# Optimization experiments

Hardware: AMD Instinct MI355X
Metric: run time of the kernel (lower is better)

Reference implementation:

```python
import jax, jax.numpy as jnp
import numpy as np

N = 8192
F_IN = 64
F_OUT = 64
ALPHA = 0.2  # LeakyReLU negative slope
NEG_INF = -9e15


def setup_inputs() -> dict:
    key = jax.random.key(0)
    k1, k2, k3, k4 = jax.random.split(key, 4)
    h = jax.random.normal(k1, (N, F_IN), dtype=jnp.float32)
    adj = jax.random.randint(k2, (N, N), 0, 2, dtype=jnp.int32)
    W = jax.random.normal(k3, (F_OUT, F_IN), dtype=jnp.float32) * (1.0 / np.sqrt(F_IN))
    a = jax.random.normal(k4, (2 * F_OUT,), dtype=jnp.float32) * (1.0 / np.sqrt(2 * F_OUT))
    return {"h": h, "adj": adj, "W": W, "a": a}


def reference(h, adj, W, a):
    # Wh = h @ W.T  (nn.Linear with no bias)
    Wh = h @ W.T  # [N, F_out]
    # The original builds [N*N, 2F] pairs then applies `a`; this is exactly
    # e_ij = leakyrelu(a1 . Wh_i + a2 . Wh_j) -- decomposed form, same math.
    a1, a2 = a[:F_OUT], a[F_OUT:]
    src = Wh @ a1  # [N]
    dst = Wh @ a2  # [N]
    e = jax.nn.leaky_relu(src[:, None] + dst[None, :], negative_slope=ALPHA)  # [N, N]
    scores = jnp.where(adj > 0, e, NEG_INF)
    attention = jax.nn.softmax(scores, axis=1)
    # dropout is identity in eval mode (dropout=0.0)
    h_prime = attention @ Wh  # [N, F_out]
    return jax.nn.elu(h_prime)
```

## Files before the change

### kernel.cpp

```cpp
#include <hip/hip_runtime.h>
#include <hip/hip_bf16.h>

#define NN 8192
#define F 64
#define ALPHA 0.2f
#define L2E 1.44269504f
#define DBOUND 16.0f
#define G 8
#define COLS (NN / G)
#define NSTEPS (COLS / 32)

typedef __attribute__((ext_vector_type(8))) short short8;
typedef __attribute__((ext_vector_type(4))) float f32x4;
typedef __attribute__((ext_vector_type(4))) int i32x4;

__device__ __forceinline__ unsigned fb(float x) {
    return __builtin_bit_cast(unsigned, x);
}
__device__ __forceinline__ short f2bf(float x) {
    union { float f; unsigned u; } v; v.f = x;
    unsigned r = v.u + 0x7FFF + ((v.u >> 16) & 1);
    return (short)(r >> 16);
}

__global__ __launch_bounds__(256) void k_prep(const float* __restrict__ h,
        const float* __restrict__ W, const float* __restrict__ a,
        short* __restrict__ WhT, float* __restrict__ src, float* __restrict__ dst2) {
    __shared__ float Wl[F][F + 1];
    __shared__ short shT[F][4];
    int tid = threadIdx.x;
    for (int m = 0; m < 4; ++m) {
        int idx = m * 1024 + tid * 4;
        float4 v = *(const float4*)&W[idx];
        int row = idx >> 6, col = idx & 63;
        Wl[row][col] = v.x; Wl[row][col + 1] = v.y;
        Wl[row][col + 2] = v.z; Wl[row][col + 3] = v.w;
    }
    __syncthreads();
    int w = tid >> 6, lane = tid & 63;
    int i = blockIdx.x * 4 + w;
    const float* hrow = &h[(size_t)i * F];
    float wh = 0.f;
    #pragma unroll
    for (int k = 0; k < F; k += 4) {
        float4 hv = *(const float4*)&hrow[k];
        wh += hv.x * Wl[lane][k] + hv.y * Wl[lane][k + 1]
            + hv.z * Wl[lane][k + 2] + hv.w * Wl[lane][k + 3];
    }
    shT[lane][w] = f2bf(wh);
    float s1 = wh * a[lane];
    float s2 = wh * a[F + lane];
    #pragma unroll
    for (int off = 32; off; off >>= 1) {
        s1 += __shfl_xor(s1, off);
        s2 += __shfl_xor(s2, off);
    }
    if (lane == 0) { src[i] = s1; dst2[i] = s2 * L2E; }
    __syncthreads();
    if (tid < F) {
        short4 v = make_short4(shT[tid][0], shT[tid][1], shT[tid][2], shT[tid][3]);
        *(short4*)&WhT[(size_t)tid * NN + blockIdx.x * 4] = v;
    }
}

__global__ __launch_bounds__(256) void k_pack(const short* __restrict__ WhT,
                                              short* __restrict__ WhTt) {
    int tid = blockIdx.x * 256 + threadIdx.x;
    int lp = tid & 63;
    int f  = (tid >> 6) & 3;
    int t  = tid >> 8;
    int row = f * 16 + (lp & 15);
    int col = t * 32 + ((lp >> 4) << 3);
    short8 v = *(const short8*)&WhT[(size_t)row * NN + col];
    *(short8*)&WhTt[(size_t)tid * 8] = v;
}

__global__ __launch_bounds__(256) void k_mask(const int* __restrict__ adj,
                                              unsigned long long* __restrict__ mg) {
    int w = threadIdx.x >> 6, l = threadIdx.x & 63;
    int gw = blockIdx.x * 4 + w;
    const int NW = 2048 * 4;
    const int NCH = (NN * NN) / 256;
    int sh = 4 * (l & 15);
    #pragma unroll 4
    for (int c = gw; c < NCH; c += NW) {
        size_t base = (size_t)c * 256;
        i32x4 a = __builtin_nontemporal_load((const i32x4*)(adj + base) + l);
        unsigned n = (a.x > 0 ? 1u : 0u) | (a.y > 0 ? 2u : 0u)
                   | (a.z > 0 ? 4u : 0u) | (a.w > 0 ? 8u : 0u);
        unsigned long long v = (unsigned long long)n << sh;
        v |= __shfl_xor(v, 1);
        v |= __shfl_xor(v, 2);
        v |= __shfl_xor(v, 4);
        v |= __shfl_xor(v, 8);
        if ((l & 15) == 0)
            mg[base / 64 + (l >> 4)] = v;
    }
}

__global__ __launch_bounds__(256, 4) void k_attn(const unsigned* __restrict__ maskg,
        const short8* __restrict__ WhTt, const float* __restrict__ src,
        const float* __restrict__ dst2,
        float* __restrict__ Opart, float* __restrict__ lpart) {
    __shared__ unsigned mlds[64][33];
    __shared__ float dlds[COLS];
    __shared__ short8 tbuf[2][256];

    int rb = blockIdx.x / G;
    int g  = blockIdx.x % G;
    int jbase = g * COLS;
    int tid = threadIdx.x;

    for (int idx = tid; idx < 64 * (COLS / 32); idx += 256) {
        int rr = idx >> 5, cc = idx & 31;
        mlds[rr][cc] = maskg[(size_t)(rb * 64 + rr) * (NN / 32) + (jbase >> 5) + cc];
    }
    for (int idx = tid; idx < COLS; idx += 256)
        dlds[idx] = dst2[jbase + idx];

    tbuf[0][tid] = WhTt[(size_t)(g * 32) * 256 + tid];

    int w = tid >> 6, lane = tid & 63;
    int r = lane & 15, q = lane >> 4;
    int qs = q * 8;
    int i = rb * 64 + w * 16 + r;

    float srcv = src[i];
    float sM = srcv + DBOUND;
    float Mi = fmaxf(sM, ALPHA * sM);
    float sL  = srcv * L2E;
    float MiL = Mi * L2E;
    float C1 = sL - MiL;
    float C2 = fmaf(sL, ALPHA, -MiL);

    f32x4 acc0{}, acc1{}, acc2{}, acc3{}, acc4{};
    short8 ones;
    #pragma unroll
    for (int k = 0; k < 8; ++k) ones[k] = (short)0x3F80;

    const unsigned* mrow = &mlds[w * 16 + r][0];

#define PEL(dv, bit, eo) { \
    float t1 = (dv) + C1; \
    float t2 = fmaf((dv), ALPHA, C2); \
    float e = __builtin_amdgcn_exp2f(fmaxf(t1, t2)); \
    eo = (bit) ? e : 0.0f; }

    for (int t = 0; t < NSTEPS; ++t) {
        __syncthreads();

        int tn = (t + 1 < NSTEPS) ? t + 1 : t;
        short8 nx = WhTt[(size_t)(g * 32 + tn) * 256 + tid];

        const short8* bp = &tbuf[t & 1][0];
        short8 b0 = bp[lane];
        short8 b1 = bp[64 + lane];
        short8 b2 = bp[128 + lane];
        short8 b3 = bp[192 + lane];

        unsigned m8 = (mrow[t] >> qs) & 0xffu;
        float4 d0 = *(const float4*)&dlds[t * 32 + qs];
        float4 d1 = *(const float4*)&dlds[t * 32 + qs + 4];

        float e0, e1, e2, e3, e4, e5, e6, e7;
        PEL(d0.x, (m8 & 1u),   e0) PEL(d0.y, (m8 & 2u),   e1)
        PEL(d0.z, (m8 & 4u),   e2) PEL(d0.w, (m8 & 8u),   e3)
        PEL(d1.x, (m8 & 16u),  e4) PEL(d1.y, (m8 & 32u),  e5)
        PEL(d1.z, (m8 & 64u),  e6) PEL(d1.w, (m8 & 128u), e7)

        unsigned w0 = __builtin_amdgcn_perm(fb(e1), fb(e0), 0x07060302u);
        unsigned w1 = __builtin_amdgcn_perm(fb(e3), fb(e2), 0x07060302u);
        unsigned w2 = __builtin_amdgcn_perm(fb(e5), fb(e4), 0x07060302u);
        unsigned w3 = __builtin_amdgcn_perm(fb(e7), fb(e6), 0x07060302u);
        short8 af = __builtin_bit_cast(short8, make_uint4(w0, w1, w2, w3));

        acc0 = __builtin_amdgcn_mfma_f32_16x16x32_bf16(af, b0, acc0, 0, 0, 0);
        acc1 = __builtin_amdgcn_mfma_f32_16x16x32_bf16(af, b1, acc1, 0, 0, 0);
        acc2 = __builtin_amdgcn_mfma_f32_16x16x32_bf16(af, b2, acc2, 0, 0, 0);
        acc3 = __builtin_amdgcn_mfma_f32_16x16x32_bf16(af, b3, acc3, 0, 0, 0);
        acc4 = __builtin_amdgcn_mfma_f32_16x16x32_bf16(af, ones, acc4, 0, 0, 0);

        tbuf[(t + 1) & 1][tid] = nx;
    }
#undef PEL

    int ic = rb * 64 + w * 16 + q * 4;
    if (r == 0) {
        #pragma unroll
        for (int reg = 0; reg < 4; ++reg)
            lpart[(size_t)g * NN + ic + reg] = acc4[reg];
    }

    size_t ob = (size_t)g * (size_t)(NN * F);
    #pragma unroll
    for (int reg = 0; reg < 4; ++reg) {
        size_t ro = ob + (size_t)(ic + reg) * F + r;
        Opart[ro]      = acc0[reg];
        Opart[ro + 16] = acc1[reg];
        Opart[ro + 32] = acc2[reg];
        Opart[ro + 48] = acc3[reg];
    }
}

__global__ __launch_bounds__(256) void k_reduce(const float* __restrict__ Opart,
        const float* __restrict__ lpart, float* __restrict__ out) {
    int idx = blockIdx.x * 256 + threadIdx.x;
    int i = idx >> 6;
    float o = 0.f, l = 0.f;
    #pragma unroll
    for (int g = 0; g < G; ++g) {
        o += Opart[(size_t)g * (NN * F) + idx];
        l += lpart[(size_t)g * NN + i];
    }
    float hp = o / l;
    out[idx] = hp > 0.f ? hp : __expf(hp) - 1.f;
}

extern "C" void kernel_launch(void* const* d_in, const int* in_sizes, int n_in,
                              void* d_out, int out_size, void* d_ws, size_t ws_size,
                              hipStream_t stream) {
    const float* h  = (const float*)d_in[0];
    const int* adj  = (const int*)d_in[1];
    const float* W  = (const float*)d_in[2];
    const float* a  = (const float*)d_in[3];
    float* out = (float*)d_out;

    char* ws = (char*)d_ws;
    const size_t OFF_WHT  = 0;
    const size_t OFF_WHTT = (1u << 20);
    const size_t OFF_SRC  = (2u << 20);
    const size_t OFF_DST  = OFF_SRC + (32u << 10);
    const size_t OFF_LP   = OFF_DST + (32u << 10);
    const size_t OFF_MASK = OFF_LP + (size_t)G * NN * 4;
    const size_t OFF_OP   = OFF_MASK + (size_t)NN * (NN / 8);

    short* WhT   = (short*)(ws + OFF_WHT);
    short* WhTt  = (short*)(ws + OFF_WHTT);
    float* src   = (float*)(ws + OFF_SRC);
    float* dst2  = (float*)(ws + OFF_DST);
    float* lpart = (float*)(ws + OFF_LP);
    unsigned long long* maskg = (unsigned long long*)(ws + OFF_MASK);
    float* Opart = (float*)(ws + OFF_OP);

    k_mask<<<2048, 256, 0, stream>>>(adj, maskg);
    k_prep<<<NN / 4, 256, 0, stream>>>(h, W, a, WhT, src, dst2);
    k_pack<<<256, 256, 0, stream>>>(WhT, WhTt);
    k_attn<<<(NN / 64) * G, 256, 0, stream>>>((const unsigned*)maskg,
                                              (const short8*)WhTt, src, dst2,
                                              Opart, lpart);
    k_reduce<<<(NN * F) / 256, 256, 0, stream>>>(Opart, lpart, out);
}
```

Measured before the change: 95.00 us.

## Fuse adjacency bitmask packing into attention kernel with double-buffered staging

Removes the separate k_mask kernel and its global bitmask buffer. The attention kernel now reads int32 adjacency directly in chunks, packs it into LDS bitmasks, and double-buffers the next chunk while computing the current one. The WhT tiles are now loaded straight from global memory into registers with one-step prefetch instead of an LDS double buffer, so the per-step barrier is replaced by one per chunk. This saves a launch and the bitmask write and re-read, but the 256MB adjacency stream must now be hidden behind the attention compute.

```diff
diff --git a/kernel.cpp b/kernel.cpp
--- a/kernel.cpp
+++ b/kernel.cpp
@@ -9,6 +9,7 @@
 #define G 8
 #define COLS (NN / G)
 #define NSTEPS (COLS / 32)
+#define NCHUNK 4
 
 typedef __attribute__((ext_vector_type(8))) short short8;
 typedef __attribute__((ext_vector_type(4))) float f32x4;
@@ -75,52 +76,40 @@
     *(short8*)&WhTt[(size_t)tid * 8] = v;
 }
 
-__global__ __launch_bounds__(256) void k_mask(const int* __restrict__ adj,
-                                              unsigned long long* __restrict__ mg) {
-    int w = threadIdx.x >> 6, l = threadIdx.x & 63;
-    int gw = blockIdx.x * 4 + w;
-    const int NW = 2048 * 4;
-    const int NCH = (NN * NN) / 256;
-    int sh = 4 * (l & 15);
-    #pragma unroll 4
-    for (int c = gw; c < NCH; c += NW) {
-        size_t base = (size_t)c * 256;
-        i32x4 a = __builtin_nontemporal_load((const i32x4*)(adj + base) + l);
-        unsigned n = (a.x > 0 ? 1u : 0u) | (a.y > 0 ? 2u : 0u)
-                   | (a.z > 0 ? 4u : 0u) | (a.w > 0 ? 8u : 0u);
-        unsigned long long v = (unsigned long long)n << sh;
-        v |= __shfl_xor(v, 1);
-        v |= __shfl_xor(v, 2);
-        v |= __shfl_xor(v, 4);
-        v |= __shfl_xor(v, 8);
-        if ((l & 15) == 0)
-            mg[base / 64 + (l >> 4)] = v;
-    }
-}
-
-__global__ __launch_bounds__(256, 4) void k_attn(const unsigned* __restrict__ maskg,
+__global__ __launch_bounds__(256, 4) void k_attn(const int* __restrict__ adj,
         const short8* __restrict__ WhTt, const float* __restrict__ src,
         const float* __restrict__ dst2,
         float* __restrict__ Opart, float* __restrict__ lpart) {
-    __shared__ unsigned mlds[64][33];
+    __shared__ unsigned mlds[2][64][9];
     __shared__ float dlds[COLS];
-    __shared__ short8 tbuf[2][256];
 
     int rb = blockIdx.x / G;
     int g  = blockIdx.x % G;
     int jbase = g * COLS;
     int tid = threadIdx.x;
-
-    for (int idx = tid; idx < 64 * (COLS / 32); idx += 256) {
-        int rr = idx >> 5, cc = idx & 31;
-        mlds[rr][cc] = maskg[(size_t)(rb * 64 + rr) * (NN / 32) + (jbase >> 5) + cc];
-    }
+    int w = tid >> 6, lane = tid & 63;
+
     for (int idx = tid; idx < COLS; idx += 256)
         dlds[idx] = dst2[jbase + idx];
 
-    tbuf[0][tid] = WhTt[(size_t)(g * 32) * 256 + tid];
-
-    int w = tid >> 6, lane = tid & 63;
+    const int* abase = adj + (size_t)(rb * 64) * NN + jbase;
+    int sh8 = 4 * (lane & 7);
+
+#define STG1(rr, c, buf) { \
+    i32x4 av = __builtin_nontemporal_load( \
+        (const i32x4*)(abase + (size_t)(rr) * NN + (c) * 256) + lane); \
+    unsigned n = (av.x > 0 ? 1u : 0u) | (av.y > 0 ? 2u : 0u) \
+               | (av.z > 0 ? 4u : 0u) | (av.w > 0 ? 8u : 0u); \
+    unsigned v = n << sh8; \
+    v |= __shfl_xor(v, 1); v |= __shfl_xor(v, 2); v |= __shfl_xor(v, 4); \
+    if ((lane & 7) == 0) mlds[buf][rr][lane >> 3] = v; }
+
+#define STAGE(c) { int _b = (c) & 1; \
+    STG1(w,      c, _b) STG1(w + 4,  c, _b) STG1(w + 8,  c, _b) STG1(w + 12, c, _b) \
+    STG1(w + 16, c, _b) STG1(w + 20, c, _b) STG1(w + 24, c, _b) STG1(w + 28, c, _b) \
+    STG1(w + 32, c, _b) STG1(w + 36, c, _b) STG1(w + 40, c, _b) STG1(w + 44, c, _b) \
+    STG1(w + 48, c, _b) STG1(w + 52, c, _b) STG1(w + 56, c, _b) STG1(w + 60, c, _b) }
+
     int r = lane & 15, q = lane >> 4;
     int qs = q * 8;
     int i = rb * 64 + w * 16 + r;
@@ -138,7 +127,9 @@
     #pragma unroll
     for (int k = 0; k < 8; ++k) ones[k] = (short)0x3F80;
 
-    const unsigned* mrow = &mlds[w * 16 + r][0];
+#define LDB(tt, B0, B1, B2, B3) { \
+    const short8* bp = WhTt + (size_t)(g * 32 + (tt)) * 256; \
+    B0 = bp[lane]; B1 = bp[64 + lane]; B2 = bp[128 + lane]; B3 = bp[192 + lane]; }
 
 #define PEL(dv, bit, eo) { \
     float t1 = (dv) + C1; \
@@ -146,43 +137,50 @@
     float e = __builtin_amdgcn_exp2f(fmaxf(t1, t2)); \
     eo = (bit) ? e : 0.0f; }
 
-    for (int t = 0; t < NSTEPS; ++t) {
+    short8 cb0, cb1, cb2, cb3, nb0, nb1, nb2, nb3;
+    LDB(0, cb0, cb1, cb2, cb3)
+    STAGE(0)
+    __syncthreads();
+
+    for (int c = 0; c < NCHUNK; ++c) {
+        if (c + 1 < NCHUNK) STAGE(c + 1)
+
+        #pragma unroll
+        for (int ts = 0; ts < 8; ++ts) {
+            int t = c * 8 + ts;
+            int tn = (t + 1 < NSTEPS) ? t + 1 : t;
+            LDB(tn, nb0, nb1, nb2, nb3)
+
+            unsigned m8 = (mlds[c & 1][w * 16 + r][ts] >> qs) & 0xffu;
+            float4 d0 = *(const float4*)&dlds[t * 32 + qs];
+            float4 d1 = *(const float4*)&dlds[t * 32 + qs + 4];
+
+            float e0, e1, e2, e3, e4, e5, e6, e7;
+            PEL(d0.x, (m8 & 1u),   e0) PEL(d0.y, (m8 & 2u),   e1)
+            PEL(d0.z, (m8 & 4u),   e2) PEL(d0.w, (m8 & 8u),   e3)
+            PEL(d1.x, (m8 & 16u),  e4) PEL(d1.y, (m8 & 32u),  e5)
+            PEL(d1.z, (m8 & 64u),  e6) PEL(d1.w, (m8 & 128u), e7)
+
+            unsigned w0 = __builtin_amdgcn_perm(fb(e1), fb(e0), 0x07060302u);
+            unsigned w1 = __builtin_amdgcn_perm(fb(e3), fb(e2), 0x07060302u);
+            unsigned w2 = __builtin_amdgcn_perm(fb(e5), fb(e4), 0x07060302u);
+            unsigned w3 = __builtin_amdgcn_perm(fb(e7), fb(e6), 0x07060302u);
+            short8 af = __builtin_bit_cast(short8, make_uint4(w0, w1, w2, w3));
+
+            acc0 = __builtin_amdgcn_mfma_f32_16x16x32_bf16(af, cb0, acc0, 0, 0, 0);
+            acc1 = __builtin_amdgcn_mfma_f32_16x16x32_bf16(af, cb1, acc1, 0, 0, 0);
+            acc2 = __builtin_amdgcn_mfma_f32_16x16x32_bf16(af, cb2, acc2, 0, 0, 0);
+            acc3 = __builtin_amdgcn_mfma_f32_16x16x32_bf16(af, cb3, acc3, 0, 0, 0);
+            acc4 = __builtin_amdgcn_mfma_f32_16x16x32_bf16(af, ones, acc4, 0, 0, 0);
+
+            cb0 = nb0; cb1 = nb1; cb2 = nb2; cb3 = nb3;
+        }
         __syncthreads();
-
-        int tn = (t + 1 < NSTEPS) ? t + 1 : t;
-        short8 nx = WhTt[(size_t)(g * 32 + tn) * 256 + tid];
-
-        const short8* bp = &tbuf[t & 1][0];
-        short8 b0 = bp[lane];
-        short8 b1 = bp[64 + lane];
-        short8 b2 = bp[128 + lane];
-        short8 b3 = bp[192 + lane];
-
-        unsigned m8 = (mrow[t] >> qs) & 0xffu;
-        float4 d0 = *(const float4*)&dlds[t * 32 + qs];
-        float4 d1 = *(const float4*)&dlds[t * 32 + qs + 4];
-
-        float e0, e1, e2, e3, e4, e5, e6, e7;
-        PEL(d0.x, (m8 & 1u),   e0) PEL(d0.y, (m8 & 2u),   e1)
-        PEL(d0.z, (m8 & 4u),   e2) PEL(d0.w, (m8 & 8u),   e3)
-        PEL(d1.x, (m8 & 16u),  e4) PEL(d1.y, (m8 & 32u),  e5)
-        PEL(d1.z, (m8 & 64u),  e6) PEL(d1.w, (m8 & 128u), e7)
-
-        unsigned w0 = __builtin_amdgcn_perm(fb(e1), fb(e0), 0x07060302u);
-        unsigned w1 = __builtin_amdgcn_perm(fb(e3), fb(e2), 0x07060302u);
-        unsigned w2 = __builtin_amdgcn_perm(fb(e5), fb(e4), 0x07060302u);
-        unsigned w3 = __builtin_amdgcn_perm(fb(e7), fb(e6), 0x07060302u);
-        short8 af = __builtin_bit_cast(short8, make_uint4(w0, w1, w2, w3));
-
-        acc0 = __builtin_amdgcn_mfma_f32_16x16x32_bf16(af, b0, acc0, 0, 0, 0);
-        acc1 = __builtin_amdgcn_mfma_f32_16x16x32_bf16(af, b1, acc1, 0, 0, 0);
-        acc2 = __builtin_amdgcn_mfma_f32_16x16x32_bf16(af, b2, acc2, 0, 0, 0);
-        acc3 = __builtin_amdgcn_mfma_f32_16x16x32_bf16(af, b3, acc3, 0, 0, 0);
-        acc4 = __builtin_amdgcn_mfma_f32_16x16x32_bf16(af, ones, acc4, 0, 0, 0);
-
-        tbuf[(t + 1) & 1][tid] = nx;
     }
 #undef PEL
+#undef LDB
+#undef STAGE
+#undef STG1
 
     int ic = rb * 64 + w * 16 + q * 4;
     if (r == 0) {
@@ -231,22 +229,18 @@
     const size_t OFF_SRC  = (2u << 20);
     const size_t OFF_DST  = OFF_SRC + (32u << 10);
     const size_t OFF_LP   = OFF_DST + (32u << 10);
-    const size_t OFF_MASK = OFF_LP + (size_t)G * NN * 4;
-    const size_t OFF_OP   = OFF_MASK + (size_t)NN * (NN / 8);
+    const size_t OFF_OP   = OFF_LP + (size_t)G * NN * 4;
 
     short* WhT   = (short*)(ws + OFF_WHT);
     short* WhTt  = (short*)(ws + OFF_WHTT);
     float* src   = (float*)(ws + OFF_SRC);
     float* dst2  = (float*)(ws + OFF_DST);
     float* lpart = (float*)(ws + OFF_LP);
-    unsigned long long* maskg = (unsigned long long*)(ws + OFF_MASK);
     float* Opart = (float*)(ws + OFF_OP);
 
-    k_mask<<<2048, 256, 0, stream>>>(adj, maskg);
     k_prep<<<NN / 4, 256, 0, stream>>>(h, W, a, WhT, src, dst2);
     k_pack<<<256, 256, 0, stream>>>(WhT, WhTt);
-    k_attn<<<(NN / 64) * G, 256, 0, stream>>>((const unsigned*)maskg,
-                                              (const short8*)WhTt, src, dst2,
+    k_attn<<<(NN / 64) * G, 256, 0, stream>>>(adj, (const short8*)WhTt, src, dst2,
                                               Opart, lpart);
     k_reduce<<<(NN * F) / 256, 256, 0, stream>>>(Opart, lpart, out);
 }
```

Measured after the change: 99.99 us. +5.2%, slower.

## Fuse mask, prep and pack kernels into one launch with direct tiled write

Applied to the files above, without the earlier changes.

Merges the adjacency bitmask kernel, the Wh projection kernel and the repack kernel into a single launch. Extra blocks handle the mask work, and prep blocks write Wh directly in the tiled MFMA layout, so the intermediate transposed buffer and its repack pass are no longer needed. This removes two launches and one global round trip of the Wh data. The two block populations now share one grid, which changes scheduling and occupancy.

```diff
diff --git a/kernel.cpp b/kernel.cpp
--- a/kernel.cpp
+++ b/kernel.cpp
@@ -23,12 +23,39 @@
     return (short)(r >> 16);
 }
 
-__global__ __launch_bounds__(256) void k_prep(const float* __restrict__ h,
+__global__ __launch_bounds__(256) void k_fused0(const float* __restrict__ h,
         const float* __restrict__ W, const float* __restrict__ a,
-        short* __restrict__ WhT, float* __restrict__ src, float* __restrict__ dst2) {
+        const int* __restrict__ adj,
+        short* __restrict__ WhTt, float* __restrict__ src,
+        float* __restrict__ dst2, unsigned long long* __restrict__ mg) {
     __shared__ float Wl[F][F + 1];
     __shared__ short shT[F][4];
     int tid = threadIdx.x;
+
+    if (blockIdx.x >= NN / 4) {
+        int bid = blockIdx.x - NN / 4;
+        int w = tid >> 6, l = tid & 63;
+        int gw = bid * 4 + w;
+        const int NW = 2048 * 4;
+        const int NCH = (NN * NN) / 256;
+        int sh = 4 * (l & 15);
+        #pragma unroll 4
+        for (int c = gw; c < NCH; c += NW) {
+            size_t base = (size_t)c * 256;
+            i32x4 av = __builtin_nontemporal_load((const i32x4*)(adj + base) + l);
+            unsigned n = (av.x > 0 ? 1u : 0u) | (av.y > 0 ? 2u : 0u)
+                       | (av.z > 0 ? 4u : 0u) | (av.w > 0 ? 8u : 0u);
+            unsigned long long v = (unsigned long long)n << sh;
+            v |= __shfl_xor(v, 1);
+            v |= __shfl_xor(v, 2);
+            v |= __shfl_xor(v, 4);
+            v |= __shfl_xor(v, 8);
+            if ((l & 15) == 0)
+                mg[base / 64 + (l >> 4)] = v;
+        }
+        return;
+    }
+
     for (int m = 0; m < 4; ++m) {
         int idx = m * 1024 + tid * 4;
         float4 v = *(const float4*)&W[idx];
@@ -58,43 +85,14 @@
     if (lane == 0) { src[i] = s1; dst2[i] = s2 * L2E; }
     __syncthreads();
     if (tid < F) {
-        short4 v = make_short4(shT[tid][0], shT[tid][1], shT[tid][2], shT[tid][3]);
-        *(short4*)&WhT[(size_t)tid * NN + blockIdx.x * 4] = v;
-    }
-}
-
-__global__ __launch_bounds__(256) void k_pack(const short* __restrict__ WhT,
-                                              short* __restrict__ WhTt) {
-    int tid = blockIdx.x * 256 + threadIdx.x;
-    int lp = tid & 63;
-    int f  = (tid >> 6) & 3;
-    int t  = tid >> 8;
-    int row = f * 16 + (lp & 15);
-    int col = t * 32 + ((lp >> 4) << 3);
-    short8 v = *(const short8*)&WhT[(size_t)row * NN + col];
-    *(short8*)&WhTt[(size_t)tid * 8] = v;
-}
-
-__global__ __launch_bounds__(256) void k_mask(const int* __restrict__ adj,
-                                              unsigned long long* __restrict__ mg) {
-    int w = threadIdx.x >> 6, l = threadIdx.x & 63;
-    int gw = blockIdx.x * 4 + w;
-    const int NW = 2048 * 4;
-    const int NCH = (NN * NN) / 256;
-    int sh = 4 * (l & 15);
-    #pragma unroll 4
-    for (int c = gw; c < NCH; c += NW) {
-        size_t base = (size_t)c * 256;
-        i32x4 a = __builtin_nontemporal_load((const i32x4*)(adj + base) + l);
-        unsigned n = (a.x > 0 ? 1u : 0u) | (a.y > 0 ? 2u : 0u)
-                   | (a.z > 0 ? 4u : 0u) | (a.w > 0 ? 8u : 0u);
-        unsigned long long v = (unsigned long long)n << sh;
-        v |= __shfl_xor(v, 1);
-        v |= __shfl_xor(v, 2);
-        v |= __shfl_xor(v, 4);
-        v |= __shfl_xor(v, 8);
-        if ((l & 15) == 0)
-            mg[base / 64 + (l >> 4)] = v;
+        int f = tid;
+        int b = blockIdx.x;
+        int t = b >> 3;
+        int off = (b * 4) & 31;
+        size_t addr = (((size_t)(t * 4 + (f >> 4)) * 64
+                       + (off >> 3) * 16 + (f & 15)) << 3) + (off & 7);
+        short4 v = make_short4(shT[f][0], shT[f][1], shT[f][2], shT[f][3]);
+        *(short4*)&WhTt[addr] = v;
     }
 }
 
@@ -226,15 +224,13 @@
     float* out = (float*)d_out;
 
     char* ws = (char*)d_ws;
-    const size_t OFF_WHT  = 0;
-    const size_t OFF_WHTT = (1u << 20);
-    const size_t OFF_SRC  = (2u << 20);
+    const size_t OFF_WHTT = 0;
+    const size_t OFF_SRC  = (1u << 20);
     const size_t OFF_DST  = OFF_SRC + (32u << 10);
     const size_t OFF_LP   = OFF_DST + (32u << 10);
     const size_t OFF_MASK = OFF_LP + (size_t)G * NN * 4;
     const size_t OFF_OP   = OFF_MASK + (size_t)NN * (NN / 8);
 
-    short* WhT   = (short*)(ws + OFF_WHT);
     short* WhTt  = (short*)(ws + OFF_WHTT);
     float* src   = (float*)(ws + OFF_SRC);
     float* dst2  = (float*)(ws + OFF_DST);
@@ -242,9 +238,7 @@
     unsigned long long* maskg = (unsigned long long*)(ws + OFF_MASK);
     float* Opart = (float*)(ws + OFF_OP);
 
-    k_mask<<<2048, 256, 0, stream>>>(adj, maskg);
-    k_prep<<<NN / 4, 256, 0, stream>>>(h, W, a, WhT, src, dst2);
-    k_pack<<<256, 256, 0, stream>>>(WhT, WhTt);
+    k_fused0<<<NN / 4 + 2048, 256, 0, stream>>>(h, W, a, adj, WhTt, src, dst2, maskg);
     k_attn<<<(NN / 64) * G, 256, 0, stream>>>((const unsigned*)maskg,
                                               (const short8*)WhTt, src, dst2,
                                               Opart, lpart);
```

New measurement: 102.3 us. +7.7%, slower.
